# Kernel optimization log

Measured on AMD Instinct MI355X. Metric: run time of the kernel, lower is better.

Reference implementation:

```python
import jax, jax.numpy as jnp
import numpy as np

D_MODEL = 1024
D_FF = 4096
LN_EPS = 1e-5


def setup_inputs() -> dict:
    key = jax.random.key(0)
    k_x, k_w1, k_w2 = jax.random.split(key, 3)
    x = jax.random.normal(k_x, (4, 2048, D_MODEL), dtype=jnp.float32)
    # LayerNorm affine params (torch defaults: weight=1, bias=0)
    ln_w = jnp.ones((D_MODEL,), dtype=jnp.float32)
    ln_b = jnp.zeros((D_MODEL,), dtype=jnp.float32)
    # Linear layers, torch default init: U(-1/sqrt(fan_in), 1/sqrt(fan_in))
    lim1 = 1.0 / np.sqrt(D_MODEL)
    w1 = jax.random.uniform(k_w1, (D_MODEL, D_FF), minval=-lim1, maxval=lim1, dtype=jnp.float32)
    b1 = jnp.zeros((D_FF,), dtype=jnp.float32)
    lim2 = 1.0 / np.sqrt(D_FF)
    w2 = jax.random.uniform(k_w2, (D_FF, D_MODEL), minval=-lim2, maxval=lim2, dtype=jnp.float32)
    b2 = jnp.zeros((D_MODEL,), dtype=jnp.float32)
    return {"x": x, "ln_w": ln_w, "ln_b": ln_b, "w1": w1, "b1": b1, "w2": w2, "b2": b2}


def reference(x, ln_w, ln_b, w1, b1, w2, b2):
    # LayerNorm over last dim
    mu = jnp.mean(x, axis=-1, keepdims=True)
    var = jnp.mean(jnp.square(x - mu), axis=-1, keepdims=True)
    h = (x - mu) * jax.lax.rsqrt(var + LN_EPS) * ln_w + ln_b
    # Linear -> ReLU -> Linear
    h = jnp.maximum(jnp.einsum('bsd,df->bsf', h, w1) + b1, 0.0)
    return jnp.einsum('bsf,fd->bsd', h, w2) + b2
```

## Files before the change

kernel.cpp:

```cpp
#include <hip/hip_runtime.h>
#include <stdint.h>

#define D_MODEL 1024
#define D_FF    4096
#define NROWS   8192

typedef __attribute__((ext_vector_type(4))) float f32x4;
typedef __attribute__((ext_vector_type(8))) short short8;

__device__ __forceinline__ unsigned short f2bf(float f) {
  unsigned u = __float_as_uint(f);
  u += 0x7fffu + ((u >> 16) & 1u);
  return (unsigned short)(u >> 16);
}

template <int N>
__device__ __forceinline__ void wait_vmcnt() {
  asm volatile("s_waitcnt vmcnt(%0)" ::"n"(N) : "memory");
}

__global__ __launch_bounds__(256) void ln_bf16_kernel(
    const float* __restrict__ x, const float* __restrict__ lnw,
    const float* __restrict__ lnb, unsigned short* __restrict__ y) {
  const int row = blockIdx.x;
  const int t = threadIdx.x;
  const int w = t >> 6, l = t & 63;
  const float4* xr = (const float4*)(x + (size_t)row * D_MODEL);
  float4 v = xr[t];
  float s  = v.x + v.y + v.z + v.w;
  float s2 = v.x * v.x + v.y * v.y + v.z * v.z + v.w * v.w;
#pragma unroll
  for (int o = 32; o >= 1; o >>= 1) {
    s  += __shfl_xor(s, o);
    s2 += __shfl_xor(s2, o);
  }
  __shared__ float red[8];
  if (l == 0) { red[w] = s; red[4 + w] = s2; }
  __syncthreads();
  s  = red[0] + red[1] + red[2] + red[3];
  s2 = red[4] + red[5] + red[6] + red[7];
  const float mu  = s * (1.0f / D_MODEL);
  const float var = s2 * (1.0f / D_MODEL) - mu * mu;
  const float rs  = rsqrtf(var + 1e-5f);
  float4 wv = ((const float4*)lnw)[t];
  float4 bv = ((const float4*)lnb)[t];
  ushort4 o4;
  o4.x = f2bf((v.x - mu) * rs * wv.x + bv.x);
  o4.y = f2bf((v.y - mu) * rs * wv.y + bv.y);
  o4.z = f2bf((v.z - mu) * rs * wv.z + bv.z);
  o4.w = f2bf((v.w - mu) * rs * wv.w + bv.w);
  *(ushort4*)(y + (size_t)row * D_MODEL + t * 4) = o4;
}

__global__ __launch_bounds__(256) void transpose_f32_bf16(
    const float* __restrict__ src, unsigned short* __restrict__ dst,
    int R, int C) {
  __shared__ float tile[32][33];
  const int tx = threadIdx.x;
  const int ty = threadIdx.y;
  const int r0 = blockIdx.y * 32, c0 = blockIdx.x * 32;
#pragma unroll
  for (int i = 0; i < 32; i += 8)
    tile[ty + i][tx] = src[(size_t)(r0 + ty + i) * C + (c0 + tx)];
  __syncthreads();
#pragma unroll
  for (int i = 0; i < 32; i += 8)
    dst[(size_t)(c0 + ty + i) * R + (r0 + tx)] = f2bf(tile[tx][ty + i]);
}

template <int BN, int RELU, int BF16OUT>
__global__ __launch_bounds__(512, 2) void gemm8s(
    const unsigned short* __restrict__ A, const unsigned short* __restrict__ Bt,
    const float* __restrict__ bias, unsigned short* __restrict__ Cb,
    float* __restrict__ Cf, int M, int N, int K) {
  constexpr int BM = 256;
  constexpr int FN = BN / 64;
  constexpr int FNH = FN / 2;
  constexpr int LA = 2;
  constexpr int LB = BN / 128;
  constexpr int AH = 128 * 64;
  constexpr int BH = (BN / 2) * 64;
  constexpr int BUFSZ = 2 * AH + 2 * BH;
  constexpr int RPW = BN / 8;
  constexpr int WTN = BN / 4;
  constexpr int NW_A = 2 * LA + LB;
  constexpr int NW_B = LA + 2 * LB;

  __shared__ short lds[2 * BUFSZ];

  const int t = threadIdx.x;
  const int w = t >> 6, l = t & 63;
  const int wm = w >> 2, wn = w & 3;
  const int lr = l & 15, lg = l >> 4, l7 = l & 7;
  const int wm64 = wm * 64, wnr = wn * RPW;

  const int gx = gridDim.x;
  const int nwg = gx * gridDim.y;
  int id = blockIdx.y * gx + blockIdx.x;
  id = (id & 7) * (nwg >> 3) + (id >> 3);
  const int bn0 = (id % gx) * BN;
  const int bm0 = (id / gx) * BM;

  f32x4 acc[8][FN];
#pragma unroll
  for (int i = 0; i < 8; ++i)
#pragma unroll
    for (int j = 0; j < FN; ++j) acc[i][j] = (f32x4){0.f, 0.f, 0.f, 0.f};

  short8 af[2][4];
  short8 bq[2][2][FNH];

  auto stageA = [&](int buf, int mq, int kt) {
#pragma unroll
    for (int i = 0; i < LA; ++i) {
      const int idx = i * 512 + t;
      const int r = idx >> 3;
      const int sl = (idx & 7) ^ (r & 7);
      const int grow = bm0 + ((r >> 6) << 7) + (mq << 6) + (r & 63);
      __builtin_amdgcn_global_load_lds(
          (const __attribute__((address_space(1))) void*)(A + (size_t)grow * K + kt * 64 + sl * 8),
          (__attribute__((address_space(3))) void*)(&lds[buf * BUFSZ + mq * AH + idx * 8]),
          16, 0, 0);
    }
  };
  auto stageB = [&](int buf, int nq, int kt) {
#pragma unroll
    for (int i = 0; i < LB; ++i) {
      const int idx = i * 512 + t;
      const int r = idx >> 3;
      const int sl = (idx & 7) ^ (r & 7);
      const int grow = bn0 + (r / RPW) * WTN + nq * RPW + (r % RPW);
      __builtin_amdgcn_global_load_lds(
          (const __attribute__((address_space(1))) void*)(Bt + (size_t)grow * K + kt * 64 + sl * 8),
          (__attribute__((address_space(3))) void*)(&lds[buf * BUFSZ + 2 * AH + nq * BH + idx * 8]),
          16, 0, 0);
    }
  };

#define PHASE(MQ, NQ, BUFR, NWAIT, LDA_, LDB_, STAGESTMT)                      \
  {                                                                            \
    wait_vmcnt<NWAIT>();                                                       \
    if (LDA_) {                                                                \
      _Pragma("unroll") for (int ks = 0; ks < 2; ++ks)                         \
        _Pragma("unroll") for (int f = 0; f < 4; ++f)                          \
          af[ks][f] = *(const short8*)&lds[(BUFR) * BUFSZ + (MQ) * AH +        \
              (wm64 + f * 16 + lr) * 64 + ((((ks << 2) | lg) ^ l7) << 3)];     \
    }                                                                          \
    if (LDB_) {                                                                \
      _Pragma("unroll") for (int ks = 0; ks < 2; ++ks)                         \
        _Pragma("unroll") for (int g = 0; g < FNH; ++g)                        \
          bq[NQ][ks][g] = *(const short8*)&lds[(BUFR) * BUFSZ + 2 * AH +       \
              (NQ) * BH + (wnr + g * 16 + lr) * 64 +                           \
              ((((ks << 2) | lg) ^ l7) << 3)];                                 \
    }                                                                          \
    STAGESTMT;                                                                 \
    __builtin_amdgcn_s_barrier();                                              \
    asm volatile("s_waitcnt lgkmcnt(0)" ::: "memory");                         \
    __builtin_amdgcn_sched_barrier(0);                                         \
    __builtin_amdgcn_s_setprio(1);                                             \
    _Pragma("unroll") for (int ks = 0; ks < 2; ++ks)                           \
      _Pragma("unroll") for (int f = 0; f < 4; ++f)                            \
        _Pragma("unroll") for (int g = 0; g < FNH; ++g)                        \
          acc[(MQ) * 4 + f][(NQ) * FNH + g] =                                  \
              __builtin_amdgcn_mfma_f32_16x16x32_bf16(                         \
                  af[ks][f], bq[NQ][ks][g], acc[(MQ) * 4 + f][(NQ) * FNH + g], \
                  0, 0, 0);                                                    \
    __builtin_amdgcn_s_setprio(0);                                             \
    __builtin_amdgcn_sched_barrier(0);                                         \
    __builtin_amdgcn_s_barrier();                                              \
  }

  const int KT_MAX = (K >> 6) - 1;
  const int NIT = K >> 7;

  stageA(0, 0, 0);
  stageB(0, 0, 0);
  stageB(0, 1, 0);
  stageA(0, 1, 0);
  stageA(1, 0, 1);
  stageB(1, 0, 1);
  wait_vmcnt<2 * LA + 2 * LB>();
  __builtin_amdgcn_s_barrier();

  for (int it = 0; it < NIT; ++it) {
    const int k1 = 2 * it + 1;
    int k2 = 2 * it + 2; k2 = k2 > KT_MAX ? KT_MAX : k2;
    int k3 = 2 * it + 3; k3 = k3 > KT_MAX ? KT_MAX : k3;
    PHASE(0, 0, 0, NW_A, 1, 1, stageB(1, 1, k1));
    PHASE(0, 1, 0, NW_B, 0, 1, stageA(1, 1, k1));
    PHASE(1, 1, 0, NW_B, 1, 0, stageA(0, 0, k2));
    PHASE(1, 0, 0, NW_A, 0, 0, stageB(0, 0, k2));
    PHASE(0, 0, 1, NW_A, 1, 1, stageB(0, 1, k2));
    PHASE(0, 1, 1, NW_B, 0, 1, stageA(0, 1, k2));
    PHASE(1, 1, 1, NW_B, 1, 0, stageA(1, 0, k3));
    PHASE(1, 0, 1, NW_A, 0, 0, stageB(1, 0, k3));
  }
#undef PHASE
  asm volatile("s_waitcnt vmcnt(0)" ::: "memory");

#pragma unroll
  for (int fn = 0; fn < FN; ++fn) {
    const int col = bn0 + wn * WTN + fn * 16 + lr;
    const float bvs = bias[col];
#pragma unroll
    for (int fm = 0; fm < 8; ++fm) {
      const int rb = bm0 + wm * 128 + fm * 16 + lg * 4;
#pragma unroll
      for (int j = 0; j < 4; ++j) {
        float v = acc[fm][fn][j] + bvs;
        if (RELU) v = v > 0.f ? v : 0.f;
        if (BF16OUT) Cb[(size_t)(rb + j) * N + col] = f2bf(v);
        else         Cf[(size_t)(rb + j) * N + col] = v;
      }
    }
  }
}

extern "C" void kernel_launch(void* const* d_in, const int* in_sizes, int n_in,
                              void* d_out, int out_size, void* d_ws, size_t ws_size,
                              hipStream_t stream) {
  const float* x   = (const float*)d_in[0];
  const float* lnw = (const float*)d_in[1];
  const float* lnb = (const float*)d_in[2];
  const float* w1  = (const float*)d_in[3];
  const float* b1  = (const float*)d_in[4];
  const float* w2  = (const float*)d_in[5];
  const float* b2  = (const float*)d_in[6];
  float* out = (float*)d_out;

  char* ws = (char*)d_ws;
  unsigned short* x_ln = (unsigned short*)(ws);
  unsigned short* w1t  = (unsigned short*)(ws + (16u << 20));
  unsigned short* w2t  = (unsigned short*)(ws + (24u << 20));
  unsigned short* h    = (unsigned short*)(ws + (32u << 20));

  ln_bf16_kernel<<<NROWS, 256, 0, stream>>>(x, lnw, lnb, x_ln);
  transpose_f32_bf16<<<dim3(D_FF / 32, D_MODEL / 32), dim3(32, 8), 0, stream>>>(
      w1, w1t, D_MODEL, D_FF);
  transpose_f32_bf16<<<dim3(D_MODEL / 32, D_FF / 32), dim3(32, 8), 0, stream>>>(
      w2, w2t, D_FF, D_MODEL);
  gemm8s<256, 1, 1><<<dim3(D_FF / 256, NROWS / 256), 512, 0, stream>>>(
      x_ln, w1t, b1, h, nullptr, NROWS, D_FF, D_MODEL);
  gemm8s<128, 0, 0><<<dim3(D_MODEL / 128, NROWS / 256), 512, 0, stream>>>(
      h, w2t, b2, nullptr, out, NROWS, D_MODEL, D_FF);
}
```

Baseline: 261.1 us.

## Specialize GEMM dims, precompute addresses, double-buffer B frags, LDS-staged bf16 epilogue

Makes N and K template constants and precomputes the global and LDS addresses used for staging and fragment reads. The B fragments for phase 0 are double-buffered (even/odd) so the next tile's read is issued a phase early. The explicit lgkmcnt wait and sched_barriers are dropped so LDS reads can overlap with MFMAs. For the bf16 output the epilogue is staged through LDS and written back as 16-byte vector stores instead of scattered 2-byte stores. This adds register pressure, and dropping the explicit waits leaves the compiler responsible for correct LDS ordering.

```diff
diff --git a/kernel.cpp b/kernel.cpp
--- a/kernel.cpp
+++ b/kernel.cpp
@@ -68,12 +68,11 @@
     dst[(size_t)(c0 + ty + i) * R + (r0 + tx)] = f2bf(tile[tx][ty + i]);
 }
 
-template <int BN, int RELU, int BF16OUT>
+template <int BN, int N_, int K_, int RELU, int BF16OUT>
 __global__ __launch_bounds__(512, 2) void gemm8s(
     const unsigned short* __restrict__ A, const unsigned short* __restrict__ Bt,
     const float* __restrict__ bias, unsigned short* __restrict__ Cb,
-    float* __restrict__ Cf, int M, int N, int K) {
-  constexpr int BM = 256;
+    float* __restrict__ Cf) {
   constexpr int FN = BN / 64;
   constexpr int FNH = FN / 2;
   constexpr int LA = 2;
@@ -87,6 +86,7 @@
   constexpr int NW_B = LA + 2 * LB;
 
   __shared__ short lds[2 * BUFSZ];
+  char* const ldsc = (char*)lds;
 
   const int t = threadIdx.x;
   const int w = t >> 6, l = t & 63;
@@ -99,7 +99,37 @@
   int id = blockIdx.y * gx + blockIdx.x;
   id = (id & 7) * (nwg >> 3) + (id >> 3);
   const int bn0 = (id % gx) * BN;
-  const int bm0 = (id / gx) * BM;
+  const int bm0 = (id / gx) * BN == 0 ? (id / gx) * 256 : (id / gx) * 256;
+
+  const unsigned short* ApB[LA];
+  int lwA[LA];
+#pragma unroll
+  for (int i = 0; i < LA; ++i) {
+    const int idx = i * 512 + t;
+    const int r = idx >> 3;
+    const int sl = (idx & 7) ^ (r & 7);
+    ApB[i] = A + (size_t)(bm0 + ((r >> 6) << 7) + (r & 63)) * K_ + (sl << 3);
+    lwA[i] = idx * 8;
+  }
+  const unsigned short* BpB[LB];
+  int lwB[LB];
+#pragma unroll
+  for (int i = 0; i < LB; ++i) {
+    const int idx = i * 512 + t;
+    const int r = idx >> 3;
+    const int sl = (idx & 7) ^ (r & 7);
+    BpB[i] = Bt + (size_t)(bn0 + (r / RPW) * WTN + (r % RPW)) * K_ + (sl << 3);
+    lwB[i] = idx * 8;
+  }
+  int aok[2][4], bok[2][FNH];
+#pragma unroll
+  for (int ks = 0; ks < 2; ++ks) {
+    const int ko = (((ks << 2) | lg) ^ l7) << 3;
+#pragma unroll
+    for (int f = 0; f < 4; ++f) aok[ks][f] = ((wm64 + f * 16 + lr) * 64 + ko) * 2;
+#pragma unroll
+    for (int g = 0; g < FNH; ++g) bok[ks][g] = ((wnr + g * 16 + lr) * 64 + ko) * 2;
+  }
 
   f32x4 acc[8][FN];
 #pragma unroll
@@ -108,70 +138,57 @@
     for (int j = 0; j < FN; ++j) acc[i][j] = (f32x4){0.f, 0.f, 0.f, 0.f};
 
   short8 af[2][4];
-  short8 bq[2][2][FNH];
+  short8 bq1[2][FNH];
+  short8 bq0e[2][FNH];
+  short8 bq0o[2][FNH];
 
   auto stageA = [&](int buf, int mq, int kt) {
 #pragma unroll
-    for (int i = 0; i < LA; ++i) {
-      const int idx = i * 512 + t;
-      const int r = idx >> 3;
-      const int sl = (idx & 7) ^ (r & 7);
-      const int grow = bm0 + ((r >> 6) << 7) + (mq << 6) + (r & 63);
+    for (int i = 0; i < LA; ++i)
       __builtin_amdgcn_global_load_lds(
-          (const __attribute__((address_space(1))) void*)(A + (size_t)grow * K + kt * 64 + sl * 8),
-          (__attribute__((address_space(3))) void*)(&lds[buf * BUFSZ + mq * AH + idx * 8]),
+          (const __attribute__((address_space(1))) void*)(ApB[i] + mq * (64 * K_) + kt * 64),
+          (__attribute__((address_space(3))) void*)(&lds[buf * BUFSZ + mq * AH + lwA[i]]),
           16, 0, 0);
-    }
   };
   auto stageB = [&](int buf, int nq, int kt) {
 #pragma unroll
-    for (int i = 0; i < LB; ++i) {
-      const int idx = i * 512 + t;
-      const int r = idx >> 3;
-      const int sl = (idx & 7) ^ (r & 7);
-      const int grow = bn0 + (r / RPW) * WTN + nq * RPW + (r % RPW);
+    for (int i = 0; i < LB; ++i)
       __builtin_amdgcn_global_load_lds(
-          (const __attribute__((address_space(1))) void*)(Bt + (size_t)grow * K + kt * 64 + sl * 8),
-          (__attribute__((address_space(3))) void*)(&lds[buf * BUFSZ + 2 * AH + nq * BH + idx * 8]),
+          (const __attribute__((address_space(1))) void*)(BpB[i] + nq * (RPW * K_) + kt * 64),
+          (__attribute__((address_space(3))) void*)(&lds[buf * BUFSZ + 2 * AH + nq * BH + lwB[i]]),
           16, 0, 0);
-    }
   };
 
-#define PHASE(MQ, NQ, BUFR, NWAIT, LDA_, LDB_, STAGESTMT)                      \
+#define RDA(BUFR, MQ)                                                          \
+  _Pragma("unroll") for (int ks = 0; ks < 2; ++ks)                             \
+    _Pragma("unroll") for (int f = 0; f < 4; ++f)                              \
+      af[ks][f] = *(const short8*)(ldsc + ((BUFR) * BUFSZ + (MQ) * AH) * 2 +   \
+                                   aok[ks][f]);
+#define RDB(DST, BUFR, NQ)                                                     \
+  _Pragma("unroll") for (int ks = 0; ks < 2; ++ks)                             \
+    _Pragma("unroll") for (int g = 0; g < FNH; ++g)                            \
+      DST[ks][g] = *(const short8*)(ldsc + ((BUFR) * BUFSZ + 2 * AH +          \
+                                            (NQ) * BH) * 2 + bok[ks][g]);
+#define PHASE(MQ, NQ, BOP, NWAIT, RDSTMT, STAGESTMT)                           \
   {                                                                            \
     wait_vmcnt<NWAIT>();                                                       \
-    if (LDA_) {                                                                \
-      _Pragma("unroll") for (int ks = 0; ks < 2; ++ks)                         \
-        _Pragma("unroll") for (int f = 0; f < 4; ++f)                          \
-          af[ks][f] = *(const short8*)&lds[(BUFR) * BUFSZ + (MQ) * AH +        \
-              (wm64 + f * 16 + lr) * 64 + ((((ks << 2) | lg) ^ l7) << 3)];     \
-    }                                                                          \
-    if (LDB_) {                                                                \
-      _Pragma("unroll") for (int ks = 0; ks < 2; ++ks)                         \
-        _Pragma("unroll") for (int g = 0; g < FNH; ++g)                        \
-          bq[NQ][ks][g] = *(const short8*)&lds[(BUFR) * BUFSZ + 2 * AH +       \
-              (NQ) * BH + (wnr + g * 16 + lr) * 64 +                           \
-              ((((ks << 2) | lg) ^ l7) << 3)];                                 \
-    }                                                                          \
+    RDSTMT;                                                                    \
     STAGESTMT;                                                                 \
     __builtin_amdgcn_s_barrier();                                              \
-    asm volatile("s_waitcnt lgkmcnt(0)" ::: "memory");                         \
-    __builtin_amdgcn_sched_barrier(0);                                         \
     __builtin_amdgcn_s_setprio(1);                                             \
     _Pragma("unroll") for (int ks = 0; ks < 2; ++ks)                           \
       _Pragma("unroll") for (int f = 0; f < 4; ++f)                            \
         _Pragma("unroll") for (int g = 0; g < FNH; ++g)                        \
           acc[(MQ) * 4 + f][(NQ) * FNH + g] =                                  \
               __builtin_amdgcn_mfma_f32_16x16x32_bf16(                         \
-                  af[ks][f], bq[NQ][ks][g], acc[(MQ) * 4 + f][(NQ) * FNH + g], \
+                  af[ks][f], BOP[ks][g], acc[(MQ) * 4 + f][(NQ) * FNH + g],    \
                   0, 0, 0);                                                    \
     __builtin_amdgcn_s_setprio(0);                                             \
-    __builtin_amdgcn_sched_barrier(0);                                         \
     __builtin_amdgcn_s_barrier();                                              \
   }
 
-  const int KT_MAX = (K >> 6) - 1;
-  const int NIT = K >> 7;
+  constexpr int KT_MAX = (K_ >> 6) - 1;
+  constexpr int NIT = K_ >> 7;
 
   stageA(0, 0, 0);
   stageB(0, 0, 0);
@@ -181,36 +198,69 @@
   stageB(1, 0, 1);
   wait_vmcnt<2 * LA + 2 * LB>();
   __builtin_amdgcn_s_barrier();
+  RDB(bq0e, 0, 0);
 
   for (int it = 0; it < NIT; ++it) {
     const int k1 = 2 * it + 1;
     int k2 = 2 * it + 2; k2 = k2 > KT_MAX ? KT_MAX : k2;
     int k3 = 2 * it + 3; k3 = k3 > KT_MAX ? KT_MAX : k3;
-    PHASE(0, 0, 0, NW_A, 1, 1, stageB(1, 1, k1));
-    PHASE(0, 1, 0, NW_B, 0, 1, stageA(1, 1, k1));
-    PHASE(1, 1, 0, NW_B, 1, 0, stageA(0, 0, k2));
-    PHASE(1, 0, 0, NW_A, 0, 0, stageB(0, 0, k2));
-    PHASE(0, 0, 1, NW_A, 1, 1, stageB(0, 1, k2));
-    PHASE(0, 1, 1, NW_B, 0, 1, stageA(0, 1, k2));
-    PHASE(1, 1, 1, NW_B, 1, 0, stageA(1, 0, k3));
-    PHASE(1, 0, 1, NW_A, 0, 0, stageB(1, 0, k3));
+    PHASE(0, 0, bq0e, NW_A, RDA(0, 0),      stageB(1, 1, k1));
+    PHASE(0, 1, bq1,  NW_B, RDB(bq1, 0, 1), stageA(1, 1, k1));
+    PHASE(1, 1, bq1,  NW_B, RDA(0, 1),      stageA(0, 0, k2));
+    PHASE(1, 0, bq0e, NW_A, RDB(bq0o, 1, 0), stageB(0, 0, k2));
+    PHASE(0, 0, bq0o, NW_A, RDA(1, 0),      stageB(0, 1, k2));
+    PHASE(0, 1, bq1,  NW_B, RDB(bq1, 1, 1), stageA(0, 1, k2));
+    PHASE(1, 1, bq1,  NW_B, RDA(1, 1),      stageA(1, 0, k3));
+    PHASE(1, 0, bq0o, NW_A, RDB(bq0e, 0, 0), stageB(1, 0, k3));
   }
 #undef PHASE
+#undef RDA
+#undef RDB
   asm volatile("s_waitcnt vmcnt(0)" ::: "memory");
 
-#pragma unroll
-  for (int fn = 0; fn < FN; ++fn) {
-    const int col = bn0 + wn * WTN + fn * 16 + lr;
-    const float bvs = bias[col];
+  if (BF16OUT) {
+    constexpr int SLP = BN + 16;
+    constexpr int TPR = BN / 8;
+    constexpr int RPR = 512 / TPR;
+    float bvs[FN];
+#pragma unroll
+    for (int fn = 0; fn < FN; ++fn) bvs[fn] = bias[bn0 + wn * WTN + fn * 16 + lr];
 #pragma unroll
     for (int fm = 0; fm < 8; ++fm) {
-      const int rb = bm0 + wm * 128 + fm * 16 + lg * 4;
-#pragma unroll
-      for (int j = 0; j < 4; ++j) {
-        float v = acc[fm][fn][j] + bvs;
-        if (RELU) v = v > 0.f ? v : 0.f;
-        if (BF16OUT) Cb[(size_t)(rb + j) * N + col] = f2bf(v);
-        else         Cf[(size_t)(rb + j) * N + col] = v;
+      __syncthreads();
+#pragma unroll
+      for (int fn = 0; fn < FN; ++fn) {
+        const int scol = wn * WTN + fn * 16 + lr;
+#pragma unroll
+        for (int j = 0; j < 4; ++j) {
+          float v = acc[fm][fn][j] + bvs[fn];
+          if (RELU) v = v > 0.f ? v : 0.f;
+          lds[(wm * 16 + lg * 4 + j) * SLP + scol] = (short)f2bf(v);
+        }
+      }
+      __syncthreads();
+#pragma unroll
+      for (int rnd = 0; rnd < 32 / RPR; ++rnd) {
+        const int ri = t / TPR + rnd * RPR;
+        const int ci = (t % TPR) * 8;
+        const int gr = bm0 + ((ri >> 4) << 7) + fm * 16 + (ri & 15);
+        *(short8*)&Cb[(size_t)gr * N_ + bn0 + ci] = *(const short8*)&lds[ri * SLP + ci];
+      }
+    }
+  } else {
+#pragma unroll
+    for (int fn = 0; fn < FN; ++fn) {
+      const int col = bn0 + wn * WTN + fn * 16 + lr;
+      const float bvs = bias[col];
+#pragma unroll
+      for (int fm = 0; fm < 8; ++fm) {
+        const int rb = bm0 + wm * 128 + fm * 16 + lg * 4;
+#pragma unroll
+        for (int j = 0; j < 4; ++j) {
+          float v = acc[fm][fn][j] + bvs;
+          if (RELU) v = v > 0.f ? v : 0.f;
+          Cf[(size_t)(rb + j) * N_ + col] = v;
+        }
       }
     }
   }
@@ -239,8 +289,8 @@
       w1, w1t, D_MODEL, D_FF);
   transpose_f32_bf16<<<dim3(D_MODEL / 32, D_FF / 32), dim3(32, 8), 0, stream>>>(
       w2, w2t, D_FF, D_MODEL);
-  gemm8s<256, 1, 1><<<dim3(D_FF / 256, NROWS / 256), 512, 0, stream>>>(
-      x_ln, w1t, b1, h, nullptr, NROWS, D_FF, D_MODEL);
-  gemm8s<128, 0, 0><<<dim3(D_MODEL / 128, NROWS / 256), 512, 0, stream>>>(
-      h, w2t, b2, nullptr, out, NROWS, D_MODEL, D_FF);
-}
+  gemm8s<256, D_FF, D_MODEL, 1, 1><<<dim3(D_FF / 256, NROWS / 256), 512, 0, stream>>>(
+      x_ln, w1t, b1, h, nullptr);
+  gemm8s<128, D_MODEL, D_FF, 0, 0><<<dim3(D_MODEL / 128, NROWS / 256), 512, 0, stream>>>(
+      h, w2t, b2, nullptr, out);
+}
```

Result: faster. 249.0 us (-4.6%).
